# Optimization experiments

Measured on AMD Instinct MI355X. Metric: run time of the kernel, lower is better.

Reference implementation:

```python
import jax, jax.numpy as jnp
import numpy as np

N_NODES = 50000
N_EDGES = 800000
D_IN = 256
D_HID = 256
D_OUT = 8


def _glorot(key, shape):
    fan_in = shape[-1]
    bound = 1.0 / np.sqrt(fan_in)
    return jax.random.uniform(key, shape, minval=-bound, maxval=bound, dtype=jnp.float32)


def setup_inputs() -> dict:
    key = jax.random.key(0)
    ks = jax.random.split(key, 12)
    x = jax.random.normal(ks[0], (N_NODES, D_IN), dtype=jnp.float32)
    edge_index = jax.random.randint(ks[1], (2, N_EDGES), 0, N_NODES, dtype=jnp.int64)
    return {
        "x": x,
        "edge_index": edge_index,
        # SAGEConv1: lin_l (neighbor path, has bias), lin_r (root path, no bias)
        "W1l": _glorot(ks[2], (D_HID, D_IN)),
        "b1": jnp.zeros((D_HID,), jnp.float32),
        "W1r": _glorot(ks[3], (D_HID, D_IN)),
        # SAGEConv2
        "W2l": _glorot(ks[4], (D_HID, D_HID)),
        "b2": jnp.zeros((D_HID,), jnp.float32),
        "W2r": _glorot(ks[5], (D_HID, D_HID)),
        # MLP decoder
        "Wm1": _glorot(ks[6], (D_HID, D_HID)),
        "bm1": _glorot(ks[7], (D_HID,)),
        "Wm2": _glorot(ks[8], (D_OUT, D_HID)),
        "bm2": _glorot(ks[9], (D_OUT,)),
    }


def _sage_conv(x, edge_index, Wl, b, Wr):
    # PyG SAGEConv with mean aggregation:
    # out = lin_l(mean_{j in N(i)} x_j) + lin_r(x_i)
    src, dst = edge_index[0], edge_index[1]
    msg = x[src]  # [E, d] gather
    agg = jax.ops.segment_sum(msg, dst, num_segments=x.shape[0])  # [N, d]
    cnt = jax.ops.segment_sum(jnp.ones((edge_index.shape[1],), x.dtype), dst,
                              num_segments=x.shape[0])  # in-degree [N]
    mean = agg / jnp.maximum(cnt, 1.0)[:, None]
    return mean @ Wl.T + b + x @ Wr.T


def reference(x, edge_index, W1l, b1, W1r, W2l, b2, W2r, Wm1, bm1, Wm2, bm2):
    h = jax.nn.relu(_sage_conv(x, edge_index, W1l, b1, W1r))
    h = jax.nn.relu(_sage_conv(h, edge_index, W2l, b2, W2r))
    h = jax.nn.relu(h @ Wm1.T + bm1)
    logits = h @ Wm2.T + bm2
    return jax.nn.softmax(logits, axis=-1)
```

## Files before the change

### kernel.cpp

```cpp
#include <hip/hip_runtime.h>
#include <math.h>

#define N_NODES 50000
#define N_EDGES 800000
#define D 256

typedef unsigned short u16;
typedef __attribute__((ext_vector_type(8))) __bf16 bf16x8;
typedef __attribute__((ext_vector_type(4))) float f32x4;

#define BUF_U16 24576
#define NBUF 3

__device__ __forceinline__ void split_hi_lo(float v, u16& h, u16& l) {
    unsigned u = __float_as_uint(v);
    unsigned hh = (u + 0x7fff + ((u >> 16) & 1)) >> 16;
    float hf = __uint_as_float(hh << 16);
    float res = v - hf;
    unsigned ul = __float_as_uint(res);
    unsigned ll = (ul + 0x7fff + ((ul >> 16) & 1)) >> 16;
    h = (u16)hh; l = (u16)ll;
}

__device__ __forceinline__ float bflo(unsigned u) { return __uint_as_float(u << 16); }
__device__ __forceinline__ float bfhi(unsigned u) { return __uint_as_float(u & 0xffff0000u); }

__device__ __forceinline__ void gl_lds16(const void* g, void* l) {
    __builtin_amdgcn_global_load_lds(
        (const __attribute__((address_space(1))) void*)g,
        (__attribute__((address_space(3))) void*)l, 16, 0, 0);
}

__global__ void count_deg(const int* __restrict__ ei, int* __restrict__ cnt) {
    int e = blockIdx.x * blockDim.x + threadIdx.x;
    if (e < N_EDGES) atomicAdd(&cnt[ei[N_EDGES + e]], 1);
}

__global__ void scan1(const int* __restrict__ cnt, int* __restrict__ partial,
                      int* __restrict__ bsum) {
    __shared__ int s[1024];
    int t = threadIdx.x, b = blockIdx.x;
    int gid = b * 1024 + t;
    int v = (gid < N_NODES) ? cnt[gid] : 0;
    s[t] = v;
    __syncthreads();
    for (int off = 1; off < 1024; off <<= 1) {
        int u = (t >= off) ? s[t - off] : 0;
        __syncthreads();
        s[t] += u;
        __syncthreads();
    }
    partial[gid] = s[t];
    if (t == 1023) bsum[b] = s[1023];
}

__global__ void scan2(const int* __restrict__ bsum, int* __restrict__ boff, int nb) {
    int t = threadIdx.x;
    int orig = (t < nb) ? bsum[t] : 0;
    int v = orig;
    #pragma unroll
    for (int off = 1; off < 64; off <<= 1) {
        int u = __shfl_up(v, off, 64);
        if (t >= off) v += u;
    }
    boff[t] = v - orig;
}

__global__ void scan3(const int* __restrict__ partial, const int* __restrict__ boff,
                      int* __restrict__ rowptr, int* __restrict__ cursor) {
    int i = blockIdx.x * blockDim.x + threadIdx.x;
    if (i <= N_NODES) {
        int val = 0;
        if (i > 0) val = partial[i - 1] + boff[(i - 1) >> 10];
        rowptr[i] = val;
        if (i < N_NODES) cursor[i] = val;
    }
}

__global__ void fill_edges(const int* __restrict__ ei, int* __restrict__ cursor,
                           int* __restrict__ esrc) {
    int e = blockIdx.x * blockDim.x + threadIdx.x;
    if (e < N_EDGES) {
        int p = atomicAdd(&cursor[ei[N_EDGES + e]], 1);
        esrc[p] = ei[e];
    }
}

#define NF_CONST (N_NODES * D)
__global__ void split_all(const float* __restrict__ x,  u16* __restrict__ xh,  u16* __restrict__ xl,
                          const float* __restrict__ w0, u16* __restrict__ w0h, u16* __restrict__ w0l,
                          const float* __restrict__ w1, u16* __restrict__ w1h, u16* __restrict__ w1l,
                          const float* __restrict__ w2, u16* __restrict__ w2h, u16* __restrict__ w2l,
                          const float* __restrict__ w3, u16* __restrict__ w3h, u16* __restrict__ w3l,
                          const float* __restrict__ w4, u16* __restrict__ w4h, u16* __restrict__ w4l) {
    int i = blockIdx.x * blockDim.x + threadIdx.x;
    const float* src; u16* dh; u16* dl; int k;
    if (i < NF_CONST) {
        src = x; dh = xh; dl = xl; k = i;
    } else {
        int r = i - NF_CONST;
        int j = r >> 16;
        k = r & 65535;
        switch (j) {
            case 0: src = w0; dh = w0h; dl = w0l; break;
            case 1: src = w1; dh = w1h; dl = w1l; break;
            case 2: src = w2; dh = w2h; dl = w2l; break;
            case 3: src = w3; dh = w3h; dl = w3l; break;
            default: if (j > 4) return;
                    src = w4; dh = w4h; dl = w4l; break;
        }
    }
    u16 h, l; split_hi_lo(src[k], h, l);
    dh[k] = h; dl[k] = l;
}

__global__ __launch_bounds__(256) void aggregate_bf16(const u16* __restrict__ in_hi,
        const int* __restrict__ rowptr, const int* __restrict__ esrc,
        u16* __restrict__ ohi, u16* __restrict__ olo) {
    int node = blockIdx.x * 4 + (threadIdx.x >> 6);
    if (node >= N_NODES) return;
    int lane = threadIdx.x & 63;
    int half = lane >> 5;
    int sub = lane & 31;
    int beg = rowptr[node], end = rowptr[node + 1];
    const u16* rowp = in_hi + sub * 8;

    float a0 = 0.f, a1 = 0.f, a2 = 0.f, a3 = 0.f;
    float a4 = 0.f, a5 = 0.f, a6 = 0.f, a7 = 0.f;

#define ACC8(v) \
    a0 += bflo(v.x); a1 += bfhi(v.x); a2 += bflo(v.y); a3 += bfhi(v.y); \
    a4 += bflo(v.z); a5 += bfhi(v.z); a6 += bflo(v.w); a7 += bfhi(v.w);

    int j = beg;
    for (; j + 16 <= end; j += 16) {
        int i0 = esrc[j +  0 + half];
        int i1 = esrc[j +  2 + half];
        int i2 = esrc[j +  4 + half];
        int i3 = esrc[j +  6 + half];
        int i4 = esrc[j +  8 + half];
        int i5 = esrc[j + 10 + half];
        int i6 = esrc[j + 12 + half];
        int i7 = esrc[j + 14 + half];
        uint4 r0 = *(const uint4*)(rowp + (size_t)i0 * D);
        uint4 r1 = *(const uint4*)(rowp + (size_t)i1 * D);
        uint4 r2 = *(const uint4*)(rowp + (size_t)i2 * D);
        uint4 r3 = *(const uint4*)(rowp + (size_t)i3 * D);
        uint4 r4 = *(const uint4*)(rowp + (size_t)i4 * D);
        uint4 r5 = *(const uint4*)(rowp + (size_t)i5 * D);
        uint4 r6 = *(const uint4*)(rowp + (size_t)i6 * D);
        uint4 r7 = *(const uint4*)(rowp + (size_t)i7 * D);
        ACC8(r0); ACC8(r1); ACC8(r2); ACC8(r3);
        ACC8(r4); ACC8(r5); ACC8(r6); ACC8(r7);
    }
    for (; j + 8 <= end; j += 8) {
        int i0 = esrc[j + 0 + half];
        int i1 = esrc[j + 2 + half];
        int i2 = esrc[j + 4 + half];
        int i3 = esrc[j + 6 + half];
        uint4 r0 = *(const uint4*)(rowp + (size_t)i0 * D);
        uint4 r1 = *(const uint4*)(rowp + (size_t)i1 * D);
        uint4 r2 = *(const uint4*)(rowp + (size_t)i2 * D);
        uint4 r3 = *(const uint4*)(rowp + (size_t)i3 * D);
        ACC8(r0); ACC8(r1); ACC8(r2); ACC8(r3);
    }
    for (; j < end; j += 2) {
        int e = j + half;
        if (e < end) {
            uint4 r = *(const uint4*)(rowp + (size_t)esrc[e] * D);
            ACC8(r);
        }
    }
#undef ACC8

    a0 += __shfl_xor(a0, 32, 64); a1 += __shfl_xor(a1, 32, 64);
    a2 += __shfl_xor(a2, 32, 64); a3 += __shfl_xor(a3, 32, 64);
    a4 += __shfl_xor(a4, 32, 64); a5 += __shfl_xor(a5, 32, 64);
    a6 += __shfl_xor(a6, 32, 64); a7 += __shfl_xor(a7, 32, 64);

    if (lane < 32) {
        float inv = 1.f / (float)max(end - beg, 1);
        float m[8] = { a0 * inv, a1 * inv, a2 * inv, a3 * inv,
                       a4 * inv, a5 * inv, a6 * inv, a7 * inv };
        u16 h[8], l[8];
        #pragma unroll
        for (int k = 0; k < 8; ++k) split_hi_lo(m[k], h[k], l[k]);
        size_t o = (size_t)node * D + lane * 8;
        *(uint4*)(ohi + o) = make_uint4(h[0] | (h[1] << 16), h[2] | (h[3] << 16),
                                        h[4] | (h[5] << 16), h[6] | (h[7] << 16));
        *(uint4*)(olo + o) = make_uint4(l[0] | (l[1] << 16), l[2] | (l[3] << 16),
                                        l[4] | (l[5] << 16), l[6] | (l[7] << 16));
    }
}

__device__ __forceinline__ void stage256(u16* buf,
        const u16* __restrict__ Ah, const u16* __restrict__ Al,
        const u16* __restrict__ Bh, const u16* __restrict__ Bl,
        int ks, int m0, int n0, int t) {
    int tr = t >> 2;
    int g  = (t & 3) ^ ((t >> 3) & 3);
    size_t boff = (size_t)(n0 + tr) * D + ks + g * 8;
    gl_lds16(Bh + boff, buf + 16384 + t * 8);
    gl_lds16(Bl + boff, buf + 20480 + t * 8);
    #pragma unroll
    for (int r = 0; r < 2; ++r) {
        int arow = m0 + r * 128 + tr; if (arow >= N_NODES) arow = N_NODES - 1;
        size_t aoff = (size_t)arow * D + ks + g * 8;
        gl_lds16(Ah + aoff, buf + r * 4096 + t * 8);
        gl_lds16(Al + aoff, buf + 8192 + r * 4096 + t * 8);
    }
}

__global__ __launch_bounds__(512, 1) void gemm_mfma(
        const u16* __restrict__ A1h, const u16* __restrict__ A1l,
        const u16* __restrict__ A2h, const u16* __restrict__ A2l,
        const u16* __restrict__ B1h, const u16* __restrict__ B1l,
        const u16* __restrict__ B2h, const u16* __restrict__ B2l,
        const float* __restrict__ bias, int K,
        u16* __restrict__ Chi, u16* __restrict__ Clo) {
    extern __shared__ u16 sh[];
    const int t = threadIdx.x;
    const int lane = t & 63;
    const int w = t >> 6;
    const int wm = (w >> 1) * 64, wn = (w & 1) * 64;

    int bid = blockIdx.x;
    int m_idx, n_idx;
    if (bid < 384) {
        m_idx = (bid >> 4) * 8 + (bid & 7);
        n_idx = (bid >> 3) & 1;
    } else {
        int r = bid - 384;
        m_idx = 192 + (r & 3);
        n_idx = r >> 2;
    }
    const int m0 = m_idx * 256, n0 = n_idx * 128;

    f32x4 acc[4][4] = {};

    const int lm = lane & 15;
    const int sw = ((lane >> 4) ^ ((lm >> 1) & 3)) * 8;
    const int nsteps = K >> 5;

    stage256(sh,           A1h, A1l, B1h, B1l,  0, m0, n0, t);
    stage256(sh + BUF_U16, A1h, A1l, B1h, B1l, 32, m0, n0, t);

    int cur = 0;
    for (int s = 0; s < nsteps; ++s) {
        if (s + 1 < nsteps) {
            asm volatile("s_waitcnt vmcnt(6)" ::: "memory");
        } else {
            asm volatile("s_waitcnt vmcnt(0)" ::: "memory");
        }
        __builtin_amdgcn_s_barrier();
        __builtin_amdgcn_sched_barrier(0);

        if (s + 2 < nsteps) {
            int sb = cur + 2; if (sb >= NBUF) sb -= NBUF;
            int ksg = (s + 2) * 32;
            if (ksg < 256) stage256(sh + sb * BUF_U16, A1h, A1l, B1h, B1l, ksg,       m0, n0, t);
            else           stage256(sh + sb * BUF_U16, A2h, A2l, B2h, B2l, ksg - 256, m0, n0, t);
        }

        const u16* buf = sh + cur * BUF_U16;
        bf16x8 ah[4], al[4], bh[4], bl[4];
        #pragma unroll
        for (int i = 0; i < 4; ++i) {
            int offA = (wm + i * 16 + lm) * 32 + sw;
            ah[i] = *(const bf16x8*)(buf + offA);
            al[i] = *(const bf16x8*)(buf + 8192 + offA);
            int offB = (wn + i * 16 + lm) * 32 + sw;
            bh[i] = *(const bf16x8*)(buf + 16384 + offB);
            bl[i] = *(const bf16x8*)(buf + 20480 + offB);
        }
        __builtin_amdgcn_s_setprio(1);
        #pragma unroll
        for (int i = 0; i < 4; ++i) {
            #pragma unroll
            for (int j = 0; j < 4; ++j) {
                acc[i][j] = __builtin_amdgcn_mfma_f32_16x16x32_bf16(ah[i], bh[j], acc[i][j], 0, 0, 0);
                acc[i][j] = __builtin_amdgcn_mfma_f32_16x16x32_bf16(ah[i], bl[j], acc[i][j], 0, 0, 0);
                acc[i][j] = __builtin_amdgcn_mfma_f32_16x16x32_bf16(al[i], bh[j], acc[i][j], 0, 0, 0);
            }
        }
        __builtin_amdgcn_s_setprio(0);

        cur = (cur == NBUF - 1) ? 0 : cur + 1;
    }

    __syncthreads();
    const int q = lane >> 4;
    #pragma unroll
    for (int j = 0; j < 4; ++j) {
        int col = wn + j * 16 + lm;
        float bb = bias[n0 + col];
        #pragma unroll
        for (int i = 0; i < 4; ++i) {
            #pragma unroll
            for (int r = 0; r < 4; ++r) {
                int row = wm + i * 16 + q * 4 + r;
                float v = fmaxf(acc[i][j][r] + bb, 0.f);
                u16 h, l; split_hi_lo(v, h, l);
                sh[row * 128 + col] = h;
                sh[32768 + row * 128 + col] = l;
            }
        }
    }
    __syncthreads();
    for (int c = t; c < 4096; c += 512) {
        int row = c >> 4;
        int off = (c & 15) * 8;
        int grow = m0 + row;
        if (grow < N_NODES) {
            size_t o = (size_t)grow * D + n0 + off;
            *(uint4*)(Chi + o) = *(const uint4*)(sh + row * 128 + off);
            *(uint4*)(Clo + o) = *(const uint4*)(sh + 32768 + row * 128 + off);
        }
    }
}

__device__ __forceinline__ void stage_mlp(u16* buf,
        const u16* __restrict__ Ah, const u16* __restrict__ Al,
        const u16* __restrict__ Bh, const u16* __restrict__ Bl,
        int ks, int m0, int t) {
    int tr = t >> 2;
    int g  = (t & 3) ^ ((t >> 3) & 3);
    int arow = m0 + tr; if (arow >= N_NODES) arow = N_NODES - 1;
    size_t aoff = (size_t)arow * D + ks + g * 8;
    gl_lds16(Ah + aoff, buf + t * 8);
    gl_lds16(Al + aoff, buf + 4096 + t * 8);
    #pragma unroll
    for (int r = 0; r < 2; ++r) {
        int u = r * 512 + t;
        int brow = u >> 2;
        int gb = (u & 3) ^ ((u >> 3) & 3);
        size_t boff = (size_t)brow * D + ks + gb * 8;
        gl_lds16(Bh + boff, buf + 8192  + u * 8);
        gl_lds16(Bl + boff, buf + 16384 + u * 8);
    }
}

__global__ __launch_bounds__(512, 1) void gemm_mlp2(
        const u16* __restrict__ Ah, const u16* __restrict__ Al,
        const u16* __restrict__ Bh, const u16* __restrict__ Bl,
        const float* __restrict__ bm1, const float* __restrict__ Wm2,
        const float* __restrict__ bm2, float* __restrict__ out) {
    extern __shared__ u16 sh[];
    const int t = threadIdx.x;
    const int lane = t & 63;
    const int w = t >> 6;
    const int wm = (w >> 2) * 64, wn = (w & 3) * 64;
    const int m0 = blockIdx.x * 128;

    f32x4 acc[4][4] = {};
    const int lm = lane & 15;
    const int sw = ((lane >> 4) ^ ((lm >> 1) & 3)) * 8;
    const int nsteps = 8;

    stage_mlp(sh,           Ah, Al, Bh, Bl,  0, m0, t);
    stage_mlp(sh + BUF_U16, Ah, Al, Bh, Bl, 32, m0, t);

    int cur = 0;
    for (int s = 0; s < nsteps; ++s) {
        if (s + 1 < nsteps) {
            asm volatile("s_waitcnt vmcnt(6)" ::: "memory");
        } else {
            asm volatile("s_waitcnt vmcnt(0)" ::: "memory");
        }
        __builtin_amdgcn_s_barrier();
        __builtin_amdgcn_sched_barrier(0);

        if (s + 2 < nsteps) {
            int sb = cur + 2; if (sb >= NBUF) sb -= NBUF;
            stage_mlp(sh + sb * BUF_U16, Ah, Al, Bh, Bl, (s + 2) * 32, m0, t);
        }

        const u16* buf = sh + cur * BUF_U16;
        bf16x8 a_h[4], a_l[4], b_h[4], b_l[4];
        #pragma unroll
        for (int i = 0; i < 4; ++i) {
            int offA = (wm + i * 16 + lm) * 32 + sw;
            a_h[i] = *(const bf16x8*)(buf + offA);
            a_l[i] = *(const bf16x8*)(buf + 4096 + offA);
            int offB = (wn + i * 16 + lm) * 32 + sw;
            b_h[i] = *(const bf16x8*)(buf + 8192 + offB);
            b_l[i] = *(const bf16x8*)(buf + 16384 + offB);
        }
        __builtin_amdgcn_s_setprio(1);
        #pragma unroll
        for (int i = 0; i < 4; ++i) {
            #pragma unroll
            for (int j = 0; j < 4; ++j) {
                acc[i][j] = __builtin_amdgcn_mfma_f32_16x16x32_bf16(a_h[i], b_h[j], acc[i][j], 0, 0, 0);
                acc[i][j] = __builtin_amdgcn_mfma_f32_16x16x32_bf16(a_h[i], b_l[j], acc[i][j], 0, 0, 0);
                acc[i][j] = __builtin_amdgcn_mfma_f32_16x16x32_bf16(a_l[i], b_h[j], acc[i][j], 0, 0, 0);
            }
        }
        __builtin_amdgcn_s_setprio(0);

        cur = (cur == NBUF - 1) ? 0 : cur + 1;
    }

    __syncthreads();
    float* h3s = (float*)sh;
    const int q = lane >> 4;
    #pragma unroll
    for (int j = 0; j < 4; ++j) {
        int col = wn + j * 16 + lm;
        float bb = bm1[col];
        #pragma unroll
        for (int i = 0; i < 4; ++i) {
            #pragma unroll
            for (int r = 0; r < 4; ++r) {
                int row = wm + i * 16 + q * 4 + r;
                h3s[row * 260 + col] = fmaxf(acc[i][j][r] + bb, 0.f);
            }
        }
    }
    __syncthreads();

    const int kl = lane & 15;
    const int sr = lane >> 4;

    float4 wreg[8][4];
    float b2v[8];
    #pragma unroll
    for (int o = 0; o < 8; ++o) {
        b2v[o] = bm2[o];
        #pragma unroll
        for (int c = 0; c < 4; ++c)
            wreg[o][c] = *(const float4*)(Wm2 + o * D + kl * 16 + c * 4);
    }

    #pragma unroll
    for (int p = 0; p < 4; ++p) {
        int row  = w * 16 + p * 4 + sr;
        int grow = m0 + row;
        const float* hrow = h3s + row * 260 + kl * 16;
        float4 h0 = *(const float4*)(hrow);
        float4 h1 = *(const float4*)(hrow + 4);
        float4 h2 = *(const float4*)(hrow + 8);
        float4 h3v = *(const float4*)(hrow + 12);
        float part[8];
        #pragma unroll
        for (int o = 0; o < 8; ++o) {
            float s;
            s  = h0.x * wreg[o][0].x + h0.y * wreg[o][0].y
               + h0.z * wreg[o][0].z + h0.w * wreg[o][0].w;
            s += h1.x * wreg[o][1].x + h1.y * wreg[o][1].y
               + h1.z * wreg[o][1].z + h1.w * wreg[o][1].w;
            s += h2.x * wreg[o][2].x + h2.y * wreg[o][2].y
               + h2.z * wreg[o][2].z + h2.w * wreg[o][2].w;
            s += h3v.x * wreg[o][3].x + h3v.y * wreg[o][3].y
               + h3v.z * wreg[o][3].z + h3v.w * wreg[o][3].w;
            part[o] = s;
        }
        #pragma unroll
        for (int o = 0; o < 8; ++o) {
            part[o] += __shfl_xor(part[o], 1, 64);
            part[o] += __shfl_xor(part[o], 2, 64);
            part[o] += __shfl_xor(part[o], 4, 64);
            part[o] += __shfl_xor(part[o], 8, 64);
        }
        float v0 = part[0] + b2v[0], v1 = part[1] + b2v[1];
        float v2 = part[2] + b2v[2], v3 = part[3] + b2v[3];
        float v4 = part[4] + b2v[4], v5 = part[5] + b2v[5];
        float v6 = part[6] + b2v[6], v7 = part[7] + b2v[7];
        float mx = fmaxf(fmaxf(fmaxf(v0, v1), fmaxf(v2, v3)),
                         fmaxf(fmaxf(v4, v5), fmaxf(v6, v7)));
        v0 = expf(v0 - mx); v1 = expf(v1 - mx); v2 = expf(v2 - mx); v3 = expf(v3 - mx);
        v4 = expf(v4 - mx); v5 = expf(v5 - mx); v6 = expf(v6 - mx); v7 = expf(v7 - mx);
        float inv = 1.f / ((v0 + v1 + v2 + v3) + (v4 + v5 + v6 + v7));
        if (kl == 0 && grow < N_NODES) {
            float4 o0 = make_float4(v0 * inv, v1 * inv, v2 * inv, v3 * inv);
            float4 o1 = make_float4(v4 * inv, v5 * inv, v6 * inv, v7 * inv);
            ((float4*)(out + (size_t)grow * 8))[0] = o0;
            ((float4*)(out + (size_t)grow * 8))[1] = o1;
        }
    }
}

static inline size_t align_up(size_t x) { return (x + 255) & ~(size_t)255; }

extern "C" void kernel_launch(void* const* d_in, const int* in_sizes, int n_in,
                              void* d_out, int out_size, void* d_ws, size_t ws_size,
                              hipStream_t stream) {
    const float* x   = (const float*)d_in[0];
    const int*   ei  = (const int*)d_in[1];
    const float* W1l = (const float*)d_in[2];
    const float* b1  = (const float*)d_in[3];
    const float* W1r = (const float*)d_in[4];
    const float* W2l = (const float*)d_in[5];
    const float* b2  = (const float*)d_in[6];
    const float* W2r = (const float*)d_in[7];
    const float* Wm1 = (const float*)d_in[8];
    const float* bm1 = (const float*)d_in[9];
    const float* Wm2 = (const float*)d_in[10];
    const float* bm2 = (const float*)d_in[11];
    float* out = (float*)d_out;

    const size_t NF = (size_t)N_NODES * D;
    const size_t NW = (size_t)D * D;

    char* w = (char*)d_ws;
    u16* x_hi  = (u16*)w; w += align_up(NF * 2);
    u16* x_lo  = (u16*)w; w += align_up(NF * 2);
    u16* mn_hi = (u16*)w; w += align_up(NF * 2 * 2);
    u16* mn_lo = mn_hi + NF;
    u16* h1_hi = (u16*)w; w += align_up(NF * 2);
    u16* h1_lo = (u16*)w; w += align_up(NF * 2);
    u16* h2_hi = (u16*)w; w += align_up(NF * 2);
    u16* h2_lo = (u16*)w; w += align_up(NF * 2);
    u16* wbuf  = (u16*)w; w += align_up(NW * 2 * 10);
    u16* w1l_h = wbuf + 0 * NW; u16* w1l_l = wbuf + 1 * NW;
    u16* w1r_h = wbuf + 2 * NW; u16* w1r_l = wbuf + 3 * NW;
    u16* w2l_h = wbuf + 4 * NW; u16* w2l_l = wbuf + 5 * NW;
    u16* w2r_h = wbuf + 6 * NW; u16* w2r_l = wbuf + 7 * NW;
    u16* wm1_h = wbuf + 8 * NW; u16* wm1_l = wbuf + 9 * NW;
    int* cnt     = (int*)w; w += align_up((size_t)N_NODES * 4);
    int* rowptr  = (int*)w; w += align_up((size_t)(N_NODES + 1) * 4);
    int* cursor  = (int*)w; w += align_up((size_t)N_NODES * 4);
    int* partial = (int*)w; w += align_up((size_t)49 * 1024 * 4);
    int* bsum    = (int*)w; w += align_up((size_t)64 * 4);
    int* boff    = (int*)w; w += align_up((size_t)64 * 4);
    int* esrc    = (int*)w; w += align_up((size_t)N_EDGES * 4);

    static bool attr_done = false;
    if (!attr_done) {
        hipFuncSetAttribute((const void*)gemm_mfma,
                            hipFuncAttributeMaxDynamicSharedMemorySize,
                            NBUF * BUF_U16 * 2);
        hipFuncSetAttribute((const void*)gemm_mlp2,
                            hipFuncAttributeMaxDynamicSharedMemorySize,
                            NBUF * BUF_U16 * 2);
        attr_done = true;
    }

    hipMemsetAsync(cnt, 0, (size_t)N_NODES * 4, stream);
    count_deg<<<(N_EDGES + 255) / 256, 256, 0, stream>>>(ei, cnt);
    scan1<<<49, 1024, 0, stream>>>(cnt, partial, bsum);
    scan2<<<1, 64, 0, stream>>>(bsum, boff, 49);
    scan3<<<(N_NODES + 256) / 256, 256, 0, stream>>>(partial, boff, rowptr, cursor);
    fill_edges<<<(N_EDGES + 255) / 256, 256, 0, stream>>>(ei, cursor, esrc);

    {
        int total = (int)(NF + 5 * NW);
        split_all<<<(total + 255) / 256, 256, 0, stream>>>(
            x,   x_hi,  x_lo,
            W1l, w1l_h, w1l_l,
            W1r, w1r_h, w1r_l,
            W2l, w2l_h, w2l_l,
            W2r, w2r_h, w2r_l,
            Wm1, wm1_h, wm1_l);
    }

    const int GEMM_LDS = NBUF * BUF_U16 * 2;
    dim3 ggrid(392);
    int agrid = (N_NODES + 3) / 4;

    aggregate_bf16<<<agrid, 256, 0, stream>>>(x_hi, rowptr, esrc, mn_hi, mn_lo);
    gemm_mfma<<<ggrid, 512, GEMM_LDS, stream>>>(mn_hi, mn_lo, x_hi, x_lo,
                                                w1l_h, w1l_l, w1r_h, w1r_l,
                                                b1, 512, h1_hi, h1_lo);
    aggregate_bf16<<<agrid, 256, 0, stream>>>(h1_hi, rowptr, esrc, mn_hi, mn_lo);
    gemm_mfma<<<ggrid, 512, GEMM_LDS, stream>>>(mn_hi, mn_lo, h1_hi, h1_lo,
                                                w2l_h, w2l_l, w2r_h, w2r_l,
                                                b2, 512, h2_hi, h2_lo);
    gemm_mlp2<<<(N_NODES + 127) / 128, 512, GEMM_LDS, stream>>>(
        h2_hi, h2_lo, wm1_h, wm1_l, bm1, Wm2, bm2, out);
}
```

Before: 480.2 us.

## Widen GEMM tile to full 256-wide N so each block reads A once

Measured after the change: 471.0 us. Within noise of the previous version (-1.9%).

```diff
diff --git a/kernel.cpp b/kernel.cpp
--- a/kernel.cpp
+++ b/kernel.cpp
@@ -8,6 +8,10 @@
 typedef unsigned short u16;
 typedef __attribute__((ext_vector_type(8))) __bf16 bf16x8;
 typedef __attribute__((ext_vector_type(4))) float f32x4;
+
+#define ABUF0 0
+#define BBUF0 49152
+#define GEMM_LDS_BYTES 163840
 
 #define BUF_U16 24576
 #define NBUF 3
@@ -193,21 +197,32 @@
     }
 }
 
-__device__ __forceinline__ void stage256(u16* buf,
+__device__ __forceinline__ void stageA256(u16* abuf,
         const u16* __restrict__ Ah, const u16* __restrict__ Al,
+        int ks, int m0, int t) {
+    #pragma unroll
+    for (int r = 0; r < 2; ++r) {
+        int u = r * 512 + t;
+        int row = u >> 2;
+        int g = (u & 3) ^ ((u >> 3) & 3);
+        int arow = m0 + row; if (arow >= N_NODES) arow = N_NODES - 1;
+        size_t off = (size_t)arow * D + ks + g * 8;
+        gl_lds16(Ah + off, abuf + u * 8);
+        gl_lds16(Al + off, abuf + 8192 + u * 8);
+    }
+}
+
+__device__ __forceinline__ void stageB256(u16* bbuf,
         const u16* __restrict__ Bh, const u16* __restrict__ Bl,
-        int ks, int m0, int n0, int t) {
-    int tr = t >> 2;
-    int g  = (t & 3) ^ ((t >> 3) & 3);
-    size_t boff = (size_t)(n0 + tr) * D + ks + g * 8;
-    gl_lds16(Bh + boff, buf + 16384 + t * 8);
-    gl_lds16(Bl + boff, buf + 20480 + t * 8);
+        int ks, int t) {
     #pragma unroll
     for (int r = 0; r < 2; ++r) {
-        int arow = m0 + r * 128 + tr; if (arow >= N_NODES) arow = N_NODES - 1;
-        size_t aoff = (size_t)arow * D + ks + g * 8;
-        gl_lds16(Ah + aoff, buf + r * 4096 + t * 8);
-        gl_lds16(Al + aoff, buf + 8192 + r * 4096 + t * 8);
+        int u = r * 512 + t;
+        int row = u >> 2;
+        int g = (u & 3) ^ ((u >> 3) & 3);
+        size_t off = (size_t)row * D + ks + g * 8;
+        gl_lds16(Bh + off, bbuf + u * 8);
+        gl_lds16(Bl + off, bbuf + 8192 + u * 8);
     }
 }
 
@@ -222,99 +237,104 @@
     const int t = threadIdx.x;
     const int lane = t & 63;
     const int w = t >> 6;
-    const int wm = (w >> 1) * 64, wn = (w & 1) * 64;
-
-    int bid = blockIdx.x;
-    int m_idx, n_idx;
-    if (bid < 384) {
-        m_idx = (bid >> 4) * 8 + (bid & 7);
-        n_idx = (bid >> 3) & 1;
-    } else {
-        int r = bid - 384;
-        m_idx = 192 + (r & 3);
-        n_idx = r >> 2;
-    }
-    const int m0 = m_idx * 256, n0 = n_idx * 128;
-
-    f32x4 acc[4][4] = {};
+    const int wm = (w >> 2) * 128, wn = (w & 3) * 64;
+    const int m0 = blockIdx.x * 256;
+
+    f32x4 acc[8][4] = {};
 
     const int lm = lane & 15;
     const int sw = ((lane >> 4) ^ ((lm >> 1) & 3)) * 8;
     const int nsteps = K >> 5;
 
-    stage256(sh,           A1h, A1l, B1h, B1l,  0, m0, n0, t);
-    stage256(sh + BUF_U16, A1h, A1l, B1h, B1l, 32, m0, n0, t);
-
-    int cur = 0;
+    stageA256(sh + ABUF0,         A1h, A1l,  0, m0, t);
+    stageB256(sh + BBUF0,         B1h, B1l,  0, t);
+    stageA256(sh + ABUF0 + 16384, A1h, A1l, 32, m0, t);
+
     for (int s = 0; s < nsteps; ++s) {
         if (s + 1 < nsteps) {
-            asm volatile("s_waitcnt vmcnt(6)" ::: "memory");
+            asm volatile("s_waitcnt vmcnt(4)" ::: "memory");
         } else {
             asm volatile("s_waitcnt vmcnt(0)" ::: "memory");
         }
         __builtin_amdgcn_s_barrier();
         __builtin_amdgcn_sched_barrier(0);
 
+        if (s + 1 < nsteps) {
+            int kk = (s + 1) * 32;
+            u16* bb = sh + BBUF0 + ((s + 1) & 1) * 16384;
+            if (kk < 256) stageB256(bb, B1h, B1l, kk, t);
+            else          stageB256(bb, B2h, B2l, kk - 256, t);
+        }
         if (s + 2 < nsteps) {
-            int sb = cur + 2; if (sb >= NBUF) sb -= NBUF;
-            int ksg = (s + 2) * 32;
-            if (ksg < 256) stage256(sh + sb * BUF_U16, A1h, A1l, B1h, B1l, ksg,       m0, n0, t);
-            else           stage256(sh + sb * BUF_U16, A2h, A2l, B2h, B2l, ksg - 256, m0, n0, t);
-        }
-
-        const u16* buf = sh + cur * BUF_U16;
-        bf16x8 ah[4], al[4], bh[4], bl[4];
-        #pragma unroll
-        for (int i = 0; i < 4; ++i) {
-            int offA = (wm + i * 16 + lm) * 32 + sw;
-            ah[i] = *(const bf16x8*)(buf + offA);
-            al[i] = *(const bf16x8*)(buf + 8192 + offA);
-            int offB = (wn + i * 16 + lm) * 32 + sw;
-            bh[i] = *(const bf16x8*)(buf + 16384 + offB);
-            bl[i] = *(const bf16x8*)(buf + 20480 + offB);
+            int kk = (s + 2) * 32;
+            u16* ab = sh + ABUF0 + ((s + 2) % 3) * 16384;
+            if (kk < 256) stageA256(ab, A1h, A1l, kk, m0, t);
+            else          stageA256(ab, A2h, A2l, kk - 256, m0, t);
+        }
+
+        const u16* ab = sh + ABUF0 + (s % 3) * 16384;
+        const u16* bb = sh + BBUF0 + (s & 1) * 16384;
+
+        bf16x8 bhf[4], blf[4];
+        #pragma unroll
+        for (int j = 0; j < 4; ++j) {
+            int offB = (wn + j * 16 + lm) * 32 + sw;
+            bhf[j] = *(const bf16x8*)(bb + offB);
+            blf[j] = *(const bf16x8*)(bb + 8192 + offB);
         }
         __builtin_amdgcn_s_setprio(1);
         #pragma unroll
-        for (int i = 0; i < 4; ++i) {
+        for (int ihalf = 0; ihalf < 2; ++ihalf) {
+            bf16x8 ahf[4], alf[4];
             #pragma unroll
-            for (int j = 0; j < 4; ++j) {
-                acc[i][j] = __builtin_amdgcn_mfma_f32_16x16x32_bf16(ah[i], bh[j], acc[i][j], 0, 0, 0);
-                acc[i][j] = __builtin_amdgcn_mfma_f32_16x16x32_bf16(ah[i], bl[j], acc[i][j], 0, 0, 0);
-                acc[i][j] = __builtin_amdgcn_mfma_f32_16x16x32_bf16(al[i], bh[j], acc[i][j], 0, 0, 0);
+            for (int ii = 0; ii < 4; ++ii) {
+                int i = ihalf * 4 + ii;
+                int offA = (wm + i * 16 + lm) * 32 + sw;
+                ahf[ii] = *(const bf16x8*)(ab + offA);
+                alf[ii] = *(const bf16x8*)(ab + 8192 + offA);
             }
+            #pragma unroll
+            for (int ii = 0; ii < 4; ++ii) {
+                int i = ihalf * 4 + ii;
+                #pragma unroll
+                for (int j = 0; j < 4; ++j) {
+                    acc[i][j] = __builtin_amdgcn_mfma_f32_16x16x32_bf16(ahf[ii], bhf[j], acc[i][j], 0, 0, 0);
+                    acc[i][j] = __builtin_amdgcn_mfma_f32_16x16x32_bf16(ahf[ii], blf[j], acc[i][j], 0, 0, 0);
+                    acc[i][j] = __builtin_amdgcn_mfma_f32_16x16x32_bf16(alf[ii], bhf[j], acc[i][j], 0, 0, 0);
+                }
+            }
         }
         __builtin_amdgcn_s_setprio(0);
-
-        cur = (cur == NBUF - 1) ? 0 : cur + 1;
-    }
-
-    __syncthreads();
+    }
+
     const int q = lane >> 4;
     #pragma unroll
-    for (int j = 0; j < 4; ++j) {
-        int col = wn + j * 16 + lm;
-        float bb = bias[n0 + col];
-        #pragma unroll
-        for (int i = 0; i < 4; ++i) {
+    for (int pl = 0; pl < 2; ++pl) {
+        __syncthreads();
+        #pragma unroll
+        for (int j = 0; j < 4; ++j) {
+            int col = wn + j * 16 + lm;
+            float bb_ = bias[col];
             #pragma unroll
-            for (int r = 0; r < 4; ++r) {
-                int row = wm + i * 16 + q * 4 + r;
-                float v = fmaxf(acc[i][j][r] + bb, 0.f);
-                u16 h, l; split_hi_lo(v, h, l);
-                sh[row * 128 + col] = h;
-                sh[32768 + row * 128 + col] = l;
+            for (int i = 0; i < 8; ++i) {
+                #pragma unroll
+                for (int r = 0; r < 4; ++r) {
+                    int row = wm + i * 16 + q * 4 + r;
+                    float v = fmaxf(acc[i][j][r] + bb_, 0.f);
+                    u16 h, l; split_hi_lo(v, h, l);
+                    sh[row * 264 + col] = pl ? l : h;
+                }
             }
         }
-    }
-    __syncthreads();
-    for (int c = t; c < 4096; c += 512) {
-        int row = c >> 4;
-        int off = (c & 15) * 8;
-        int grow = m0 + row;
-        if (grow < N_NODES) {
-            size_t o = (size_t)grow * D + n0 + off;
-            *(uint4*)(Chi + o) = *(const uint4*)(sh + row * 128 + off);
-            *(uint4*)(Clo + o) = *(const uint4*)(sh + 32768 + row * 128 + off);
+        __syncthreads();
+        u16* dst = pl ? Clo : Chi;
+        for (int c = t; c < 8192; c += 512) {
+            int row = c >> 5;
+            int off = (c & 31) * 8;
+            int grow = m0 + row;
+            if (grow < N_NODES)
+                *(uint4*)(dst + (size_t)grow * D + off) =
+                    *(const uint4*)(sh + row * 264 + off);
         }
     }
 }
@@ -529,7 +549,7 @@
     if (!attr_done) {
         hipFuncSetAttribute((const void*)gemm_mfma,
                             hipFuncAttributeMaxDynamicSharedMemorySize,
-                            NBUF * BUF_U16 * 2);
+                            GEMM_LDS_BYTES);
         hipFuncSetAttribute((const void*)gemm_mlp2,
                             hipFuncAttributeMaxDynamicSharedMemorySize,
                             NBUF * BUF_U16 * 2);
@@ -554,18 +574,17 @@
             Wm1, wm1_h, wm1_l);
     }
 
-    const int GEMM_LDS = NBUF * BUF_U16 * 2;
-    dim3 ggrid(392);
+    dim3 ggrid((N_NODES + 255) / 256);
     int agrid = (N_NODES + 3) / 4;
 
     aggregate_bf16<<<agrid, 256, 0, stream>>>(x_hi, rowptr, esrc, mn_hi, mn_lo);
-    gemm_mfma<<<ggrid, 512, GEMM_LDS, stream>>>(mn_hi, mn_lo, x_hi, x_lo,
-                                                w1l_h, w1l_l, w1r_h, w1r_l,
-                                                b1, 512, h1_hi, h1_lo);
+    gemm_mfma<<<ggrid, 512, GEMM_LDS_BYTES, stream>>>(mn_hi, mn_lo, x_hi, x_lo,
+                                                      w1l_h, w1l_l, w1r_h, w1r_l,
+                                                      b1, 512, h1_hi, h1_lo);
     aggregate_bf16<<<agrid, 256, 0, stream>>>(h1_hi, rowptr, esrc, mn_hi, mn_lo);
-    gemm_mfma<<<ggrid, 512, GEMM_LDS, stream>>>(mn_hi, mn_lo, h1_hi, h1_lo,
-                                                w2l_h, w2l_l, w2r_h, w2r_l,
-                                                b2, 512, h2_hi, h2_lo);
-    gemm_mlp2<<<(N_NODES + 127) / 128, 512, GEMM_LDS, stream>>>(
+    gemm_mfma<<<ggrid, 512, GEMM_LDS_BYTES, stream>>>(mn_hi, mn_lo, h1_hi, h1_lo,
+                                                      w2l_h, w2l_l, w2r_h, w2r_l,
+                                                      b2, 512, h2_hi, h2_lo);
+    gemm_mlp2<<<(N_NODES + 127) / 128, 512, NBUF * BUF_U16 * 2, stream>>>(
         h2_hi, h2_lo, wm1_h, wm1_l, bm1, Wm2, bm2, out);
 }
```
